# Performance work log

Measured on AMD Instinct MI355X. Metric: run time of the kernel, lower is better.

Reference implementation:

```python
import jax, jax.numpy as jnp
import numpy as np

T, N, I, R, O = 512, 1024, 64, 256, 1  # inter_size == recurrent_size == R


def setup_inputs() -> dict:
    key = jax.random.key(0)
    ks = jax.random.split(key, 13)
    s = 0.05
    return {
        "inputs": jax.random.normal(ks[0], (T, N, I), dtype=jnp.float32),
        # hiddenPrep: Linear(R, R)
        "Whp": jax.random.normal(ks[1], (R, R), jnp.float32) * s,
        "bhp": jax.random.normal(ks[2], (R,), jnp.float32) * s,
        # currentPrep: Linear(I, R)  (inter_size == R)
        "Wcp": jax.random.normal(ks[3], (I, R), jnp.float32) * s,
        "bcp": jax.random.normal(ks[4], (R,), jnp.float32) * s,
        # meshup: Linear(2R, R)
        "Wm": jax.random.normal(ks[5], (2 * R, R), jnp.float32) * s,
        "bm": jax.random.normal(ks[6], (R,), jnp.float32) * s,
        # hiddenPost: Linear(R, R)
        "Whpost": jax.random.normal(ks[7], (R, R), jnp.float32) * s,
        "bhpost": jax.random.normal(ks[8], (R,), jnp.float32) * s,
        "Wr1": jax.random.normal(ks[9], (R, R), jnp.float32) * s,
        "br1": jax.random.normal(ks[10], (R,), jnp.float32) * s,
        "Wr2": jax.random.normal(ks[11], (R, O), jnp.float32) * s,
        "br2": jax.random.normal(ks[12], (O,), jnp.float32) * s,
    }


def reference(inputs, Whp, bhp, Wcp, bcp, Wm, bm, Whpost, bhpost, Wr1, br1, Wr2, br2):
    n, r = inputs.shape[1], Whp.shape[0]

    def step(h, x):
        # RCell_complex: tanh(hiddenPost(tanh(meshup(tanh(cat[hiddenPrep(h), currentPrep(x)])))))
        cat = jnp.tanh(jnp.concatenate([h @ Whp + bhp, x @ Wcp + bcp], axis=-1))  # [N, 2R]
        h_new = jnp.tanh(jnp.tanh(cat @ Wm + bm) @ Whpost + bhpost)  # [N, R]
        out = jax.nn.relu(h_new @ Wr1 + br1) @ Wr2 + br2  # [N, O]
        return h_new, out

    h0 = jnp.zeros((n, r), dtype=inputs.dtype)
    _, outs = jax.lax.scan(step, h0, inputs)  # outs: [T, N, O]
    return outs
```

## Files before the change

kernel.cpp:

```cpp
#include <hip/hip_runtime.h>
#include <hip/hip_bf16.h>

#define TT 512
#define NB 1024

typedef float f32x4 __attribute__((ext_vector_type(4)));
typedef __bf16 bf16x8 __attribute__((ext_vector_type(8)));

#define OFF_HP 0
#define OFF_CP 65536
#define OFF_M  81920
#define OFF_PO 212992
#define OFF_R1 278528
#define TOT    344064

#define H_OFF_BYTES (1u << 20)
#define H_ELEMS ((size_t)TT * 64 * 8 * 512)

#define KEEP(v) asm volatile("" : "+v"(v))

__device__ __forceinline__ bf16x8 as_bf(const f32x4 v) {
  union U { f32x4 f; bf16x8 b; } u; u.f = v; return u.b;
}

__global__ __launch_bounds__(256) void pack_weights(
    const float* __restrict__ Whp, const float* __restrict__ Wm,
    const float* __restrict__ Wcp, const float* __restrict__ Whpost,
    const float* __restrict__ Wr1, __bf16* __restrict__ wsp) {
  int id = blockIdx.x * 256 + threadIdx.x;
  if (id >= TOT) return;
  int j = id & 7, lane = (id >> 3) & 63;
  int lq = lane >> 4, l15 = lane & 15;
  int rel, KT; const float* W; bool perm = true;
  if (id < OFF_CP)      { rel = id;          KT = 8;  W = Whp; }
  else if (id < OFF_M)  { rel = id - OFF_CP; KT = 2;  W = Wcp; perm = false; }
  else if (id < OFF_PO) { rel = id - OFF_M;  KT = 16; W = Wm; }
  else if (id < OFF_R1) { rel = id - OFF_PO; KT = 8;  W = Whpost; }
  else                  { rel = id - OFF_R1; KT = 8;  W = Wr1; }
  int ktm = rel >> 9;
  int kt = ktm % KT, mt = ktm / KT;
  int phi = 16 * mt + l15;
  int kk;
  if (perm) {
    int kb = (kt >= 8) ? kt - 8 : kt;
    kk = 32 * kb + 16 * (j >> 2) + 4 * lq + (j & 3);
    if (kt >= 8) kk += 256;
  } else {
    kk = 32 * kt + 8 * lq + j;
  }
  wsp[id] = (__bf16)W[kk * 256 + phi];
}

__device__ __forceinline__ float tanh_fast(float x) {
  float t = __expf(2.0f * x);
  return 1.0f - __fdividef(2.0f, t + 1.0f);
}

#define MFMA(a, b, c) __builtin_amdgcn_mfma_f32_16x16x32_bf16((a), (b), (c), 0, 0, 0)

__device__ __forceinline__ bf16x8 pack2(__bf16* region, int wv, int lane,
                                        const f32x4& a0, const f32x4& a1) {
  bf16x8 f;
  #pragma unroll
  for (int r = 0; r < 4; ++r) {
    f[r]     = (__bf16)tanh_fast(a0[r]);
    f[4 + r] = (__bf16)tanh_fast(a1[r]);
  }
  *(bf16x8*)(region + wv * 512 + lane * 8) = f;
  return f;
}

__device__ __forceinline__ void barrier_lds() {
  asm volatile("s_waitcnt lgkmcnt(0)" ::: "memory");
  __builtin_amdgcn_s_barrier();
  asm volatile("" ::: "memory");
}

__global__ __launch_bounds__(512)
__attribute__((amdgpu_waves_per_eu(2, 2)))
void rnn_seq_a(
    const float* __restrict__ x, const __bf16* __restrict__ wsp,
    __bf16* __restrict__ hist,
    const float* __restrict__ bhp, const float* __restrict__ bcp,
    const float* __restrict__ bm, const float* __restrict__ bhpost) {
  __shared__ __align__(16) __bf16 hB[8 * 512];
  __shared__ __align__(16) __bf16 mB[16 * 512];
  __shared__ __align__(16) __bf16 uB[8 * 512];
  __shared__ __align__(16) __bf16 wmcL[112 * 512];
  __shared__ float lb[4 * 256];

  const int tid  = threadIdx.x;
  const int wv   = tid >> 6;
  const int lane = tid & 63;
  const int lq   = lane >> 4, l15 = lane & 15;
  const int n0   = blockIdx.x * 16;
  const int mt0  = 2 * wv;

  if (tid < 256) {
    lb[0 * 256 + tid] = bhp[tid];
    lb[1 * 256 + tid] = bcp[tid];
    lb[2 * 256 + tid] = bm[tid];
    lb[3 * 256 + tid] = bhpost[tid];
  }
  for (int i = tid; i < 8 * 512; i += 512) hB[i] = (__bf16)0.0f;

  for (int v = tid; v < 112 * 64; v += 512) {
    int frag = v >> 6, lp = v & 63;
    int mt = frag / 7, c = frag - mt * 7;
    ((bf16x8*)wmcL)[v] =
        *(const bf16x8*)(wsp + OFF_M + (size_t)(mt * 16 + 8 + c) * 512 + lp * 8);
  }

  #define BIAS(a, m) (*(const f32x4*)(lb + (a) * 256 + (m) * 16 + 4 * lq))

  f32x4 hpw[16], wmh[16];
  {
    const __bf16* hp0 = wsp + OFF_HP + (size_t)(mt0 * 8) * 512 + lane * 8;
    const __bf16* mp  = wsp + OFF_M + (size_t)(mt0 * 16) * 512 + lane * 8;
    #pragma unroll
    for (int i = 0; i < 16; ++i) hpw[i] = *(const f32x4*)(hp0 + i * 512);
    #pragma unroll
    for (int kt = 0; kt < 8; ++kt) {
      wmh[kt]     = *(const f32x4*)(mp + kt * 512);
      wmh[8 + kt] = *(const f32x4*)(mp + (16 + kt) * 512);
    }
  }
  #pragma unroll
  for (int i = 0; i < 16; ++i) { KEEP(hpw[i]); KEEP(wmh[i]); }

  const __bf16* cp_p   = wsp + OFF_CP + (size_t)(mt0 * 2) * 512 + lane * 8;
  const __bf16* po_p   = wsp + OFF_PO + (size_t)(mt0 * 8) * 512 + lane * 8;
  const __bf16* wmk15a = wsp + OFF_M + (size_t)(mt0 * 16 + 15) * 512 + lane * 8;
  const __bf16* wmk15b = wsp + OFF_M + (size_t)((mt0 + 1) * 16 + 15) * 512 + lane * 8;
  const __bf16* wc0 = wmcL + (size_t)(mt0 * 7) * 512 + lane * 8;
  const __bf16* wc1 = wmcL + (size_t)((mt0 + 1) * 7) * 512 + lane * 8;
  __bf16* hst = hist + (size_t)(blockIdx.x * 8 + wv) * 512 + lane * 8;

  __syncthreads();

  const float* xbase = x + (size_t)(n0 + l15) * 64 + 8 * lq;
  f32x4 xr0 = *(const f32x4*)(xbase);
  f32x4 xr1 = *(const f32x4*)(xbase + 4);
  f32x4 xr2 = *(const f32x4*)(xbase + 32);
  f32x4 xr3 = *(const f32x4*)(xbase + 36);

  for (int t = 0; t < TT; ++t) {
    bf16x8 Bx0, Bx1;
    #pragma unroll
    for (int j = 0; j < 4; ++j) {
      Bx0[j] = (__bf16)xr0[j]; Bx0[4 + j] = (__bf16)xr1[j];
      Bx1[j] = (__bf16)xr2[j]; Bx1[4 + j] = (__bf16)xr3[j];
    }

    bf16x8 cpb[4];
    #pragma unroll
    for (int p = 0; p < 4; ++p) cpb[p] = *(const bf16x8*)(cp_p + p * 512);
    bf16x8 wk15a = *(const bf16x8*)(wmk15a);
    bf16x8 wk15b = *(const bf16x8*)(wmk15b);
    bf16x8 Bh[8];
    #pragma unroll
    for (int kt = 0; kt < 8; ++kt)
      Bh[kt] = *(const bf16x8*)(hB + kt * 512 + lane * 8);

    f32x4 ah0 = BIAS(0, mt0), ah1 = BIAS(0, mt0 + 1);
    #pragma unroll
    for (int i = 0; i < 16; ++i) {
      bf16x8 a = as_bf(hpw[i]);
      if (i < 8) ah0 = MFMA(a, Bh[i & 7], ah0);
      else       ah1 = MFMA(a, Bh[i & 7], ah1);
    }
    f32x4 ac0 = BIAS(1, mt0), ac1 = BIAS(1, mt0 + 1);
    ac0 = MFMA(cpb[0], Bx0, ac0); ac0 = MFMA(cpb[1], Bx1, ac0);
    ac1 = MFMA(cpb[2], Bx0, ac1); ac1 = MFMA(cpb[3], Bx1, ac1);

    pack2(mB,           wv, lane, ah0, ah1);
    pack2(mB + 8 * 512, wv, lane, ac0, ac1);
    barrier_lds();

    f32x4 am0 = BIAS(2, mt0), am1 = BIAS(2, mt0 + 1);
    #pragma unroll
    for (int i = 0; i < 16; ++i) {
      bf16x8 Bm = *(const bf16x8*)(mB + i * 512 + lane * 8);
      bf16x8 w0, w1;
      if (i < 8)       { w0 = as_bf(wmh[i]); w1 = as_bf(wmh[8 + i]); }
      else if (i < 15) { w0 = *(const bf16x8*)(wc0 + (i - 8) * 512);
                         w1 = *(const bf16x8*)(wc1 + (i - 8) * 512); }
      else             { w0 = wk15a; w1 = wk15b; }
      am0 = MFMA(w0, Bm, am0);
      am1 = MFMA(w1, Bm, am1);
    }
    bf16x8 pob[8];
    #pragma unroll
    for (int p = 0; p < 8; ++p) pob[p] = *(const bf16x8*)(po_p + p * 512);
    {
      int tn = (t + 1 < TT) ? t + 1 : TT - 1;
      const float* xp = xbase + (size_t)tn * NB * 64;
      xr0 = *(const f32x4*)(xp);      xr1 = *(const f32x4*)(xp + 4);
      xr2 = *(const f32x4*)(xp + 32); xr3 = *(const f32x4*)(xp + 36);
    }
    pack2(uB, wv, lane, am0, am1);
    barrier_lds();

    bf16x8 Bu[8];
    #pragma unroll
    for (int kt = 0; kt < 8; ++kt)
      Bu[kt] = *(const bf16x8*)(uB + kt * 512 + lane * 8);
    f32x4 ap0 = BIAS(3, mt0), ap1 = BIAS(3, mt0 + 1);
    #pragma unroll
    for (int i = 0; i < 16; ++i) {
      bf16x8 a = pob[i & 7];
      if (i < 8) ap0 = MFMA(a, Bu[i & 7], ap0);
      else       ap1 = MFMA(a, Bu[i & 7], ap1);
      if (i + 8 < 16) pob[i & 7] = *(const bf16x8*)(po_p + (i + 8) * 512);
    }
    bf16x8 f = pack2(hB, wv, lane, ap0, ap1);
    *(bf16x8*)(hst + (size_t)t * (64 * 8 * 512)) = f;
    barrier_lds();
  }
  #undef BIAS
}

__global__ __launch_bounds__(512) void head_out(
    const __bf16* __restrict__ wsp, const __bf16* __restrict__ hist,
    const float* __restrict__ br1, const float* __restrict__ Wr2,
    const float* __restrict__ br2, float* __restrict__ out) {
  __shared__ float outp[128];
  const int tid  = threadIdx.x;
  const int wv   = tid >> 6;
  const int lane = tid & 63;
  const int lq   = lane >> 4;
  const int t    = blockIdx.x;
  const int mt0  = 2 * wv;

  f32x4 r1w[16];
  {
    const __bf16* r1p = wsp + OFF_R1 + (size_t)(mt0 * 8) * 512 + lane * 8;
    #pragma unroll
    for (int i = 0; i < 16; ++i) r1w[i] = *(const f32x4*)(r1p + i * 512);
  }
  #pragma unroll
  for (int i = 0; i < 16; ++i) KEEP(r1w[i]);

  const f32x4 w2a = *(const f32x4*)(Wr2 + mt0 * 16 + 4 * lq);
  const f32x4 w2b = *(const f32x4*)(Wr2 + (mt0 + 1) * 16 + 4 * lq);
  const f32x4 b0  = *(const f32x4*)(br1 + mt0 * 16 + 4 * lq);
  const f32x4 b1  = *(const f32x4*)(br1 + (mt0 + 1) * 16 + 4 * lq);
  const float br2v = br2[0];

  for (int nb = 0; nb < 64; ++nb) {
    const __bf16* hp = hist + (size_t)((t * 64 + nb) * 8) * 512 + lane * 8;
    bf16x8 Bh[8];
    #pragma unroll
    for (int k = 0; k < 8; ++k) Bh[k] = *(const bf16x8*)(hp + k * 512);
    f32x4 ar0 = b0, ar1 = b1;
    #pragma unroll
    for (int i = 0; i < 16; ++i) {
      if (i < 8) ar0 = MFMA(as_bf(r1w[i]), Bh[i], ar0);
      else       ar1 = MFMA(as_bf(r1w[i]), Bh[i - 8], ar1);
    }
    float p = 0.f;
    #pragma unroll
    for (int r = 0; r < 4; ++r)
      p += fmaxf(ar0[r], 0.f) * w2a[r] + fmaxf(ar1[r], 0.f) * w2b[r];
    p += __shfl_xor(p, 16, 64);
    p += __shfl_xor(p, 32, 64);
    if (lane < 16) outp[wv * 16 + lane] = p;
    __syncthreads();
    if (tid < 16) {
      float s = br2v;
      #pragma unroll
      for (int w = 0; w < 8; ++w) s += outp[w * 16 + tid];
      out[(size_t)t * NB + nb * 16 + tid] = s;
    }
    __syncthreads();
  }
}

__global__ __launch_bounds__(512)
__attribute__((amdgpu_waves_per_eu(2, 2)))
void rnn_seq(
    const float* __restrict__ x, const __bf16* __restrict__ wsp,
    const float* __restrict__ bhp, const float* __restrict__ bcp,
    const float* __restrict__ bm, const float* __restrict__ bhpost,
    const float* __restrict__ br1, const float* __restrict__ Wr2,
    const float* __restrict__ br2, float* __restrict__ out) {
  __shared__ __align__(16) __bf16 hB[8 * 512];
  __shared__ __align__(16) __bf16 mB[16 * 512];
  __shared__ __align__(16) __bf16 uB[8 * 512];
  __shared__ __align__(16) __bf16 r1L[112 * 512];
  __shared__ float lb[5 * 256];
  __shared__ float outp[128];

  const int tid  = threadIdx.x;
  const int wv   = tid >> 6;
  const int lane = tid & 63;
  const int lq   = lane >> 4, l15 = lane & 15;
  const int n0   = blockIdx.x * 16;
  const int mt0  = 2 * wv;

  if (tid < 256) {
    lb[0 * 256 + tid] = bhp[tid];
    lb[1 * 256 + tid] = bcp[tid];
    lb[2 * 256 + tid] = bm[tid];
    lb[3 * 256 + tid] = bhpost[tid];
    lb[4 * 256 + tid] = br1[tid];
  }
  for (int i = tid; i < 8 * 512; i += 512) hB[i] = (__bf16)0.0f;

  for (int v = tid; v < 112 * 64; v += 512) {
    int frag = v >> 6, lp = v & 63;
    int mt = frag / 7, kt = frag - mt * 7;
    ((bf16x8*)r1L)[v] =
        *(const bf16x8*)(wsp + OFF_R1 + (size_t)(mt * 8 + kt) * 512 + lp * 8);
  }
  const float br2v = br2[0];

  #define BIAS(a, m) (*(const f32x4*)(lb + (a) * 256 + (m) * 16 + 4 * lq))
  const f32x4 w2a = *(const f32x4*)(Wr2 + mt0 * 16 + 4 * lq);
  const f32x4 w2b = *(const f32x4*)(Wr2 + (mt0 + 1) * 16 + 4 * lq);

  f32x4 wm0f[16]; bf16x8 wm1[16];
  {
    const __bf16* mp = wsp + OFF_M + (size_t)(mt0 * 16) * 512 + lane * 8;
    #pragma unroll
    for (int kt = 0; kt < 16; ++kt) {
      wm0f[kt] = *(const f32x4*)(mp + kt * 512);
      wm1[kt]  = *(const bf16x8*)(mp + (16 + kt) * 512);
    }
  }
  #pragma unroll
  for (int i = 0; i < 16; ++i) KEEP(wm0f[i]);

  const __bf16* hp_p = wsp + OFF_HP + (size_t)(mt0 * 8) * 512 + lane * 8;
  const __bf16* r1_p = wsp + OFF_R1 + (size_t)(mt0 * 8) * 512 + lane * 8;
  const __bf16* cp_p = wsp + OFF_CP + (size_t)(mt0 * 2) * 512 + lane * 8;
  const __bf16* po_p = wsp + OFF_PO + (size_t)(mt0 * 8) * 512 + lane * 8;
  const __bf16* r1Lp = r1L + (size_t)(mt0 * 7) * 512 + lane * 8;

  __syncthreads();

  const float* xbase = x + (size_t)(n0 + l15) * 64 + 8 * lq;
  f32x4 xr0 = *(const f32x4*)(xbase);
  f32x4 xr1 = *(const f32x4*)(xbase + 4);
  f32x4 xr2 = *(const f32x4*)(xbase + 32);
  f32x4 xr3 = *(const f32x4*)(xbase + 36);

  bf16x8 hpb[8];
  #pragma unroll
  for (int p = 0; p < 8; ++p) hpb[p] = *(const bf16x8*)(hp_p + p * 512);

  for (int t = 0; t < TT; ++t) {
    if (t >= 2 && tid < 16) {
      float s = br2v;
      #pragma unroll
      for (int w = 0; w < 8; ++w) s += outp[w * 16 + tid];
      out[(size_t)(t - 2) * NB + n0 + tid] = s;
    }

    bf16x8 Bx0, Bx1;
    #pragma unroll
    for (int j = 0; j < 4; ++j) {
      Bx0[j] = (__bf16)xr0[j]; Bx0[4 + j] = (__bf16)xr1[j];
      Bx1[j] = (__bf16)xr2[j]; Bx1[4 + j] = (__bf16)xr3[j];
    }

    bf16x8 cpb[4];
    #pragma unroll
    for (int p = 0; p < 4; ++p) cpb[p] = *(const bf16x8*)(cp_p + p * 512);
    bf16x8 r1k7a = *(const bf16x8*)(r1_p + 7 * 512);
    bf16x8 r1k7b = *(const bf16x8*)(r1_p + 15 * 512);
    bf16x8 Bh[8];
    #pragma unroll
    for (int kt = 0; kt < 8; ++kt)
      Bh[kt] = *(const bf16x8*)(hB + kt * 512 + lane * 8);

    f32x4 ah0 = BIAS(0, mt0), ah1 = BIAS(0, mt0 + 1);
    #pragma unroll
    for (int i = 0; i < 16; ++i) {
      bf16x8 a = hpb[i & 7];
      if (i < 8) ah0 = MFMA(a, Bh[i & 7], ah0);
      else       ah1 = MFMA(a, Bh[i & 7], ah1);
      if (i + 8 < 16) hpb[i & 7] = *(const bf16x8*)(hp_p + (i + 8) * 512);
    }
    f32x4 ac0 = BIAS(1, mt0), ac1 = BIAS(1, mt0 + 1);
    ac0 = MFMA(cpb[0], Bx0, ac0); ac0 = MFMA(cpb[1], Bx1, ac0);
    ac1 = MFMA(cpb[2], Bx0, ac1); ac1 = MFMA(cpb[3], Bx1, ac1);

    pack2(mB,           wv, lane, ah0, ah1);
    pack2(mB + 8 * 512, wv, lane, ac0, ac1);
    barrier_lds();

    f32x4 am0 = BIAS(2, mt0), am1 = BIAS(2, mt0 + 1);
    f32x4 ar0 = BIAS(4, mt0), ar1 = BIAS(4, mt0 + 1);
    #pragma unroll
    for (int i = 0; i < 16; ++i) {
      bf16x8 Bm = *(const bf16x8*)(mB + i * 512 + lane * 8);
      am0 = MFMA(as_bf(wm0f[i]), Bm, am0);
      am1 = MFMA(wm1[i], Bm, am1);
      int k = i & 7;
      bf16x8 a;
      if (k < 7) a = *(const bf16x8*)(r1Lp + ((i >> 3) * 7 + k) * 512);
      else       a = (i < 8) ? r1k7a : r1k7b;
      if (i < 8) ar0 = MFMA(a, Bh[k], ar0);
      else       ar1 = MFMA(a, Bh[k], ar1);
    }
    bf16x8 pob[8];
    #pragma unroll
    for (int p = 0; p < 8; ++p) pob[p] = *(const bf16x8*)(po_p + p * 512);
    {
      int tn = (t + 1 < TT) ? t + 1 : TT - 1;
      const float* xp = xbase + (size_t)tn * NB * 64;
      xr0 = *(const f32x4*)(xp);      xr1 = *(const f32x4*)(xp + 4);
      xr2 = *(const f32x4*)(xp + 32); xr3 = *(const f32x4*)(xp + 36);
    }
    pack2(uB, wv, lane, am0, am1);
    barrier_lds();

    #pragma unroll
    for (int p = 0; p < 8; ++p) hpb[p] = *(const bf16x8*)(hp_p + p * 512);
    bf16x8 Bu[8];
    #pragma unroll
    for (int kt = 0; kt < 8; ++kt)
      Bu[kt] = *(const bf16x8*)(uB + kt * 512 + lane * 8);
    {
      float p = 0.f;
      #pragma unroll
      for (int r = 0; r < 4; ++r)
        p += fmaxf(ar0[r], 0.f) * w2a[r] + fmaxf(ar1[r], 0.f) * w2b[r];
      p += __shfl_xor(p, 16, 64);
      p += __shfl_xor(p, 32, 64);
      if (lane < 16) outp[wv * 16 + lane] = p;
    }
    f32x4 ap0 = BIAS(3, mt0), ap1 = BIAS(3, mt0 + 1);
    #pragma unroll
    for (int i = 0; i < 16; ++i) {
      bf16x8 a = pob[i & 7];
      if (i < 8) ap0 = MFMA(a, Bu[i & 7], ap0);
      else       ap1 = MFMA(a, Bu[i & 7], ap1);
      if (i + 8 < 16) pob[i & 7] = *(const bf16x8*)(po_p + (i + 8) * 512);
    }
    pack2(hB, wv, lane, ap0, ap1);
    barrier_lds();
  }

  if (tid < 16) {
    float s = br2v;
    #pragma unroll
    for (int w = 0; w < 8; ++w) s += outp[w * 16 + tid];
    out[(size_t)(TT - 2) * NB + n0 + tid] = s;
  }
  barrier_lds();

  {
    bf16x8 Bh[8];
    #pragma unroll
    for (int kt = 0; kt < 8; ++kt)
      Bh[kt] = *(const bf16x8*)(hB + kt * 512 + lane * 8);
    f32x4 ar0 = BIAS(4, mt0), ar1 = BIAS(4, mt0 + 1);
    bf16x8 r1b[8];
    #pragma unroll
    for (int p = 0; p < 8; ++p) r1b[p] = *(const bf16x8*)(r1_p + p * 512);
    #pragma unroll
    for (int i = 0; i < 16; ++i) {
      bf16x8 a = r1b[i & 7];
      if (i < 8) ar0 = MFMA(a, Bh[i & 7], ar0);
      else       ar1 = MFMA(a, Bh[i & 7], ar1);
      if (i + 8 < 16) r1b[i & 7] = *(const bf16x8*)(r1_p + (i + 8) * 512);
    }
    float p = 0.f;
    #pragma unroll
    for (int r = 0; r < 4; ++r)
      p += fmaxf(ar0[r], 0.f) * w2a[r] + fmaxf(ar1[r], 0.f) * w2b[r];
    p += __shfl_xor(p, 16, 64);
    p += __shfl_xor(p, 32, 64);
    if (lane < 16) outp[wv * 16 + lane] = p;
    barrier_lds();
    if (tid < 16) {
      float s = br2v;
      #pragma unroll
      for (int w = 0; w < 8; ++w) s += outp[w * 16 + tid];
      out[(size_t)(TT - 1) * NB + n0 + tid] = s;
    }
  }
  #undef BIAS
}

extern "C" void kernel_launch(void* const* d_in, const int* in_sizes, int n_in,
                              void* d_out, int out_size, void* d_ws, size_t ws_size,
                              hipStream_t stream) {
  const float* x      = (const float*)d_in[0];
  const float* Whp    = (const float*)d_in[1];
  const float* bhp    = (const float*)d_in[2];
  const float* Wcp    = (const float*)d_in[3];
  const float* bcp    = (const float*)d_in[4];
  const float* Wm     = (const float*)d_in[5];
  const float* bm     = (const float*)d_in[6];
  const float* Whpost = (const float*)d_in[7];
  const float* bhpost = (const float*)d_in[8];
  const float* Wr1    = (const float*)d_in[9];
  const float* br1    = (const float*)d_in[10];
  const float* Wr2    = (const float*)d_in[11];
  const float* br2    = (const float*)d_in[12];
  __bf16* wsp = (__bf16*)d_ws;
  float*  out = (float*)d_out;

  if (ws_size < (size_t)TOT * sizeof(__bf16)) return;

  pack_weights<<<(TOT + 255) / 256, 256, 0, stream>>>(Whp, Wm, Wcp, Whpost, Wr1, wsp);

  const size_t H_BYTES = H_ELEMS * sizeof(__bf16);
  if (ws_size >= (size_t)H_OFF_BYTES + H_BYTES) {
    __bf16* hist = (__bf16*)((char*)d_ws + H_OFF_BYTES);
    rnn_seq_a<<<64, 512, 0, stream>>>(x, wsp, hist, bhp, bcp, bm, bhpost);
    head_out<<<TT, 512, 0, stream>>>(wsp, hist, br1, Wr2, br2, out);
  } else {
    rnn_seq<<<64, 512, 0, stream>>>(x, wsp, bhp, bcp, bm, bhpost, br1, Wr2,
                                    br2, out);
  }
}
```

Before: 2.832 ms.

## Halve recurrent block to 4 waves holding all weights in registers; split head grid

The sequential RNN kernel now runs with 256 threads, and each wave computes four output tiles instead of two. All hiddenPrep, meshup and currentPrep weight fragments are kept in registers (about 416 VGPRs' worth, using AGPRs), which removes the LDS-resident meshup weights and the per-step global weight loads. Each h/m/x fragment read from LDS is also reused across four MFMAs. The head kernel gets a second grid dimension so each block handles a quarter of the batch, and the fallback kernel's prefetch is moved. The trade-off is fewer waves for latency hiding, heavy register pressure and possible spills.

Result: slower. 4.964 ms (+75.3%).

```diff
diff --git a/kernel.cpp b/kernel.cpp
--- a/kernel.cpp
+++ b/kernel.cpp
@@ -58,7 +58,7 @@
 
 #define MFMA(a, b, c) __builtin_amdgcn_mfma_f32_16x16x32_bf16((a), (b), (c), 0, 0, 0)
 
-__device__ __forceinline__ bf16x8 pack2(__bf16* region, int wv, int lane,
+__device__ __forceinline__ bf16x8 pack2(__bf16* region, int fr, int lane,
                                         const f32x4& a0, const f32x4& a1) {
   bf16x8 f;
   #pragma unroll
@@ -66,7 +66,7 @@
     f[r]     = (__bf16)tanh_fast(a0[r]);
     f[4 + r] = (__bf16)tanh_fast(a1[r]);
   }
-  *(bf16x8*)(region + wv * 512 + lane * 8) = f;
+  *(bf16x8*)(region + fr * 512 + lane * 8) = f;
   return f;
 }
 
@@ -76,9 +76,9 @@
   asm volatile("" ::: "memory");
 }
 
-__global__ __launch_bounds__(512)
-__attribute__((amdgpu_waves_per_eu(2, 2)))
-void rnn_seq_a(
+__global__ __launch_bounds__(256)
+__attribute__((amdgpu_waves_per_eu(1, 1)))
+void rnn_seq_c(
     const float* __restrict__ x, const __bf16* __restrict__ wsp,
     __bf16* __restrict__ hist,
     const float* __restrict__ bhp, const float* __restrict__ bcp,
@@ -86,7 +86,6 @@
   __shared__ __align__(16) __bf16 hB[8 * 512];
   __shared__ __align__(16) __bf16 mB[16 * 512];
   __shared__ __align__(16) __bf16 uB[8 * 512];
-  __shared__ __align__(16) __bf16 wmcL[112 * 512];
   __shared__ float lb[4 * 256];
 
   const int tid  = threadIdx.x;
@@ -94,7 +93,8 @@
   const int lane = tid & 63;
   const int lq   = lane >> 4, l15 = lane & 15;
   const int n0   = blockIdx.x * 16;
-  const int mt0  = 2 * wv;
+  const int mt0  = 4 * wv;
+  const int f0   = 2 * wv;
 
   if (tid < 256) {
     lb[0 * 256 + tid] = bhp[tid];
@@ -102,39 +102,34 @@
     lb[2 * 256 + tid] = bm[tid];
     lb[3 * 256 + tid] = bhpost[tid];
   }
-  for (int i = tid; i < 8 * 512; i += 512) hB[i] = (__bf16)0.0f;
-
-  for (int v = tid; v < 112 * 64; v += 512) {
-    int frag = v >> 6, lp = v & 63;
-    int mt = frag / 7, c = frag - mt * 7;
-    ((bf16x8*)wmcL)[v] =
-        *(const bf16x8*)(wsp + OFF_M + (size_t)(mt * 16 + 8 + c) * 512 + lp * 8);
-  }
+  for (int i = tid; i < 8 * 512; i += 256) hB[i] = (__bf16)0.0f;
 
   #define BIAS(a, m) (*(const f32x4*)(lb + (a) * 256 + (m) * 16 + 4 * lq))
 
-  f32x4 hpw[16], wmh[16];
+  f32x4 hpw[32], wmw[64], cpw[8];
   {
-    const __bf16* hp0 = wsp + OFF_HP + (size_t)(mt0 * 8) * 512 + lane * 8;
-    const __bf16* mp  = wsp + OFF_M + (size_t)(mt0 * 16) * 512 + lane * 8;
-    #pragma unroll
-    for (int i = 0; i < 16; ++i) hpw[i] = *(const f32x4*)(hp0 + i * 512);
-    #pragma unroll
-    for (int kt = 0; kt < 8; ++kt) {
-      wmh[kt]     = *(const f32x4*)(mp + kt * 512);
-      wmh[8 + kt] = *(const f32x4*)(mp + (16 + kt) * 512);
-    }
-  }
-  #pragma unroll
-  for (int i = 0; i < 16; ++i) { KEEP(hpw[i]); KEEP(wmh[i]); }
-
-  const __bf16* cp_p   = wsp + OFF_CP + (size_t)(mt0 * 2) * 512 + lane * 8;
-  const __bf16* po_p   = wsp + OFF_PO + (size_t)(mt0 * 8) * 512 + lane * 8;
-  const __bf16* wmk15a = wsp + OFF_M + (size_t)(mt0 * 16 + 15) * 512 + lane * 8;
-  const __bf16* wmk15b = wsp + OFF_M + (size_t)((mt0 + 1) * 16 + 15) * 512 + lane * 8;
-  const __bf16* wc0 = wmcL + (size_t)(mt0 * 7) * 512 + lane * 8;
-  const __bf16* wc1 = wmcL + (size_t)((mt0 + 1) * 7) * 512 + lane * 8;
-  __bf16* hst = hist + (size_t)(blockIdx.x * 8 + wv) * 512 + lane * 8;
+    #pragma unroll
+    for (int mt = 0; mt < 4; ++mt) {
+      const __bf16* hp0 = wsp + OFF_HP + (size_t)((mt0 + mt) * 8) * 512 + lane * 8;
+      const __bf16* mm0 = wsp + OFF_M  + (size_t)((mt0 + mt) * 16) * 512 + lane * 8;
+      const __bf16* cc0 = wsp + OFF_CP + (size_t)((mt0 + mt) * 2) * 512 + lane * 8;
+      #pragma unroll
+      for (int kt = 0; kt < 8; ++kt)  hpw[mt * 8 + kt]  = *(const f32x4*)(hp0 + kt * 512);
+      #pragma unroll
+      for (int i = 0; i < 16; ++i)    wmw[mt * 16 + i]  = *(const f32x4*)(mm0 + i * 512);
+      #pragma unroll
+      for (int k = 0; k < 2; ++k)     cpw[mt * 2 + k]   = *(const f32x4*)(cc0 + k * 512);
+    }
+  }
+  #pragma unroll
+  for (int i = 0; i < 32; ++i) KEEP(hpw[i]);
+  #pragma unroll
+  for (int i = 0; i < 64; ++i) KEEP(wmw[i]);
+  #pragma unroll
+  for (int i = 0; i < 8; ++i)  KEEP(cpw[i]);
+
+  const __bf16* po_p = wsp + OFF_PO + (size_t)(mt0 * 8) * 512 + lane * 8;
+  __bf16* hst = hist + (size_t)(blockIdx.x * 8 + f0) * 512 + lane * 8;
 
   __syncthreads();
 
@@ -152,69 +147,78 @@
       Bx1[j] = (__bf16)xr2[j]; Bx1[4 + j] = (__bf16)xr3[j];
     }
 
-    bf16x8 cpb[4];
-    #pragma unroll
-    for (int p = 0; p < 4; ++p) cpb[p] = *(const bf16x8*)(cp_p + p * 512);
-    bf16x8 wk15a = *(const bf16x8*)(wmk15a);
-    bf16x8 wk15b = *(const bf16x8*)(wmk15b);
-    bf16x8 Bh[8];
-    #pragma unroll
-    for (int kt = 0; kt < 8; ++kt)
-      Bh[kt] = *(const bf16x8*)(hB + kt * 512 + lane * 8);
-
-    f32x4 ah0 = BIAS(0, mt0), ah1 = BIAS(0, mt0 + 1);
-    #pragma unroll
-    for (int i = 0; i < 16; ++i) {
-      bf16x8 a = as_bf(hpw[i]);
-      if (i < 8) ah0 = MFMA(a, Bh[i & 7], ah0);
-      else       ah1 = MFMA(a, Bh[i & 7], ah1);
-    }
-    f32x4 ac0 = BIAS(1, mt0), ac1 = BIAS(1, mt0 + 1);
-    ac0 = MFMA(cpb[0], Bx0, ac0); ac0 = MFMA(cpb[1], Bx1, ac0);
-    ac1 = MFMA(cpb[2], Bx0, ac1); ac1 = MFMA(cpb[3], Bx1, ac1);
-
-    pack2(mB,           wv, lane, ah0, ah1);
-    pack2(mB + 8 * 512, wv, lane, ac0, ac1);
-    barrier_lds();
-
-    f32x4 am0 = BIAS(2, mt0), am1 = BIAS(2, mt0 + 1);
-    #pragma unroll
-    for (int i = 0; i < 16; ++i) {
-      bf16x8 Bm = *(const bf16x8*)(mB + i * 512 + lane * 8);
-      bf16x8 w0, w1;
-      if (i < 8)       { w0 = as_bf(wmh[i]); w1 = as_bf(wmh[8 + i]); }
-      else if (i < 15) { w0 = *(const bf16x8*)(wc0 + (i - 8) * 512);
-                         w1 = *(const bf16x8*)(wc1 + (i - 8) * 512); }
-      else             { w0 = wk15a; w1 = wk15b; }
-      am0 = MFMA(w0, Bm, am0);
-      am1 = MFMA(w1, Bm, am1);
-    }
+    f32x4 ah[4];
+    #pragma unroll
+    for (int mt = 0; mt < 4; ++mt) ah[mt] = BIAS(0, mt0 + mt);
+    #pragma unroll
+    for (int kt = 0; kt < 8; ++kt) {
+      bf16x8 bh = *(const bf16x8*)(hB + kt * 512 + lane * 8);
+      #pragma unroll
+      for (int mt = 0; mt < 4; ++mt)
+        ah[mt] = MFMA(as_bf(hpw[mt * 8 + kt]), bh, ah[mt]);
+    }
+    f32x4 ac[4];
+    #pragma unroll
+    for (int mt = 0; mt < 4; ++mt) {
+      ac[mt] = BIAS(1, mt0 + mt);
+      ac[mt] = MFMA(as_bf(cpw[mt * 2 + 0]), Bx0, ac[mt]);
+      ac[mt] = MFMA(as_bf(cpw[mt * 2 + 1]), Bx1, ac[mt]);
+    }
+    pack2(mB,           f0,     lane, ah[0], ah[1]);
+    pack2(mB,           f0 + 1, lane, ah[2], ah[3]);
+    pack2(mB + 8 * 512, f0,     lane, ac[0], ac[1]);
+    pack2(mB + 8 * 512, f0 + 1, lane, ac[2], ac[3]);
+    barrier_lds();
+
     bf16x8 pob[8];
     #pragma unroll
-    for (int p = 0; p < 8; ++p) pob[p] = *(const bf16x8*)(po_p + p * 512);
+    for (int c = 0; c < 8; ++c) {
+      int g = (c & 3) * 8 + (c >> 2);
+      pob[c] = *(const bf16x8*)(po_p + g * 512);
+    }
     {
       int tn = (t + 1 < TT) ? t + 1 : TT - 1;
       const float* xp = xbase + (size_t)tn * NB * 64;
       xr0 = *(const f32x4*)(xp);      xr1 = *(const f32x4*)(xp + 4);
       xr2 = *(const f32x4*)(xp + 32); xr3 = *(const f32x4*)(xp + 36);
     }
-    pack2(uB, wv, lane, am0, am1);
-    barrier_lds();
-
-    bf16x8 Bu[8];
-    #pragma unroll
-    for (int kt = 0; kt < 8; ++kt)
-      Bu[kt] = *(const bf16x8*)(uB + kt * 512 + lane * 8);
-    f32x4 ap0 = BIAS(3, mt0), ap1 = BIAS(3, mt0 + 1);
+    f32x4 am[4];
+    #pragma unroll
+    for (int mt = 0; mt < 4; ++mt) am[mt] = BIAS(2, mt0 + mt);
     #pragma unroll
     for (int i = 0; i < 16; ++i) {
-      bf16x8 a = pob[i & 7];
-      if (i < 8) ap0 = MFMA(a, Bu[i & 7], ap0);
-      else       ap1 = MFMA(a, Bu[i & 7], ap1);
-      if (i + 8 < 16) pob[i & 7] = *(const bf16x8*)(po_p + (i + 8) * 512);
-    }
-    bf16x8 f = pack2(hB, wv, lane, ap0, ap1);
-    *(bf16x8*)(hst + (size_t)t * (64 * 8 * 512)) = f;
+      bf16x8 bmv = *(const bf16x8*)(mB + i * 512 + lane * 8);
+      #pragma unroll
+      for (int mt = 0; mt < 4; ++mt)
+        am[mt] = MFMA(as_bf(wmw[mt * 16 + i]), bmv, am[mt]);
+    }
+    pack2(uB, f0,     lane, am[0], am[1]);
+    pack2(uB, f0 + 1, lane, am[2], am[3]);
+    barrier_lds();
+
+    f32x4 ap[4];
+    #pragma unroll
+    for (int mt = 0; mt < 4; ++mt) ap[mt] = BIAS(3, mt0 + mt);
+    #pragma unroll
+    for (int kt = 0; kt < 8; ++kt) {
+      bf16x8 bu = *(const bf16x8*)(uB + kt * 512 + lane * 8);
+      #pragma unroll
+      for (int mt = 0; mt < 4; ++mt) {
+        int c = kt * 4 + mt;
+        ap[mt] = MFMA(pob[c & 7], bu, ap[mt]);
+        if (c + 8 < 32) {
+          int g = ((c + 8) & 3) * 8 + ((c + 8) >> 2);
+          pob[c & 7] = *(const bf16x8*)(po_p + g * 512);
+        }
+      }
+    }
+    bf16x8 h0 = pack2(hB, f0,     lane, ap[0], ap[1]);
+    bf16x8 h1 = pack2(hB, f0 + 1, lane, ap[2], ap[3]);
+    {
+      __bf16* hw = hst + (size_t)t * (64 * 8 * 512);
+      *(bf16x8*)(hw)       = h0;
+      *(bf16x8*)(hw + 512) = h1;
+    }
     barrier_lds();
   }
   #undef BIAS
@@ -230,6 +234,7 @@
   const int lane = tid & 63;
   const int lq   = lane >> 4;
   const int t    = blockIdx.x;
+  const int nb0  = blockIdx.y * 16;
   const int mt0  = 2 * wv;
 
   f32x4 r1w[16];
@@ -247,7 +252,7 @@
   const f32x4 b1  = *(const f32x4*)(br1 + (mt0 + 1) * 16 + 4 * lq);
   const float br2v = br2[0];
 
-  for (int nb = 0; nb < 64; ++nb) {
+  for (int nb = nb0; nb < nb0 + 16; ++nb) {
     const __bf16* hp = hist + (size_t)((t * 64 + nb) * 8) * 512 + lane * 8;
     bf16x8 Bh[8];
     #pragma unroll
@@ -416,8 +421,6 @@
     pack2(uB, wv, lane, am0, am1);
     barrier_lds();
 
-    #pragma unroll
-    for (int p = 0; p < 8; ++p) hpb[p] = *(const bf16x8*)(hp_p + p * 512);
     bf16x8 Bu[8];
     #pragma unroll
     for (int kt = 0; kt < 8; ++kt)
@@ -440,6 +443,8 @@
       if (i + 8 < 16) pob[i & 7] = *(const bf16x8*)(po_p + (i + 8) * 512);
     }
     pack2(hB, wv, lane, ap0, ap1);
+    #pragma unroll
+    for (int p = 0; p < 8; ++p) hpb[p] = *(const bf16x8*)(hp_p + p * 512);
     barrier_lds();
   }
 
@@ -511,8 +516,8 @@
   const size_t H_BYTES = H_ELEMS * sizeof(__bf16);
   if (ws_size >= (size_t)H_OFF_BYTES + H_BYTES) {
     __bf16* hist = (__bf16*)((char*)d_ws + H_OFF_BYTES);
-    rnn_seq_a<<<64, 512, 0, stream>>>(x, wsp, hist, bhp, bcp, bm, bhpost);
-    head_out<<<TT, 512, 0, stream>>>(wsp, hist, br1, Wr2, br2, out);
+    rnn_seq_c<<<64, 256, 0, stream>>>(x, wsp, hist, bhp, bcp, bm, bhpost);
+    head_out<<<dim3(TT, 4), 512, 0, stream>>>(wsp, hist, br1, Wr2, br2, out);
   } else {
     rnn_seq<<<64, 512, 0, stream>>>(x, wsp, bhp, bcp, bm, bhpost, br1, Wr2,
                                     br2, out);
```

## Double-buffer head loads, widen head grid, and hoist hiddenPost weight loads

Applied to the files above, without the earlier changes.

The head kernel now splits each timestep's 64 batch tiles across 8 blocks in a second grid dimension. Each block double-buffers its hidden-state loads so the next tile's global reads overlap the current tile's MFMA work. In the recurrent kernel, all 16 hiddenPost weight fragments are fetched earlier (half before the meshup MFMAs) instead of being streamed inside the MFMA loop, which raises register pressure. The fallback kernel moves its hiddenPrep weight reload to before the final barrier.

Result: slower. 2.984 ms (+5.4%).

```diff
diff --git a/kernel.cpp b/kernel.cpp
--- a/kernel.cpp
+++ b/kernel.cpp
@@ -58,7 +58,7 @@
 
 #define MFMA(a, b, c) __builtin_amdgcn_mfma_f32_16x16x32_bf16((a), (b), (c), 0, 0, 0)
 
-__device__ __forceinline__ bf16x8 pack2(__bf16* region, int wv, int lane,
+__device__ __forceinline__ bf16x8 pack2(__bf16* region, int fr, int lane,
                                         const f32x4& a0, const f32x4& a1) {
   bf16x8 f;
   #pragma unroll
@@ -66,7 +66,7 @@
     f[r]     = (__bf16)tanh_fast(a0[r]);
     f[4 + r] = (__bf16)tanh_fast(a1[r]);
   }
-  *(bf16x8*)(region + wv * 512 + lane * 8) = f;
+  *(bf16x8*)(region + fr * 512 + lane * 8) = f;
   return f;
 }
 
@@ -177,6 +177,10 @@
     pack2(mB + 8 * 512, wv, lane, ac0, ac1);
     barrier_lds();
 
+    bf16x8 pob[16];
+    #pragma unroll
+    for (int p = 0; p < 8; ++p) pob[p] = *(const bf16x8*)(po_p + p * 512);
+
     f32x4 am0 = BIAS(2, mt0), am1 = BIAS(2, mt0 + 1);
     #pragma unroll
     for (int i = 0; i < 16; ++i) {
@@ -189,9 +193,8 @@
       am0 = MFMA(w0, Bm, am0);
       am1 = MFMA(w1, Bm, am1);
     }
-    bf16x8 pob[8];
-    #pragma unroll
-    for (int p = 0; p < 8; ++p) pob[p] = *(const bf16x8*)(po_p + p * 512);
+    #pragma unroll
+    for (int p = 8; p < 16; ++p) pob[p] = *(const bf16x8*)(po_p + p * 512);
     {
       int tn = (t + 1 < TT) ? t + 1 : TT - 1;
       const float* xp = xbase + (size_t)tn * NB * 64;
@@ -208,10 +211,9 @@
     f32x4 ap0 = BIAS(3, mt0), ap1 = BIAS(3, mt0 + 1);
     #pragma unroll
     for (int i = 0; i < 16; ++i) {
-      bf16x8 a = pob[i & 7];
+      bf16x8 a = pob[i];
       if (i < 8) ap0 = MFMA(a, Bu[i & 7], ap0);
       else       ap1 = MFMA(a, Bu[i & 7], ap1);
-      if (i + 8 < 16) pob[i & 7] = *(const bf16x8*)(po_p + (i + 8) * 512);
     }
     bf16x8 f = pack2(hB, wv, lane, ap0, ap1);
     *(bf16x8*)(hst + (size_t)t * (64 * 8 * 512)) = f;
@@ -230,6 +232,7 @@
   const int lane = tid & 63;
   const int lq   = lane >> 4;
   const int t    = blockIdx.x;
+  const int nb0  = blockIdx.y * 8;
   const int mt0  = 2 * wv;
 
   f32x4 r1w[16];
@@ -247,33 +250,48 @@
   const f32x4 b1  = *(const f32x4*)(br1 + (mt0 + 1) * 16 + 4 * lq);
   const float br2v = br2[0];
 
-  for (int nb = 0; nb < 64; ++nb) {
-    const __bf16* hp = hist + (size_t)((t * 64 + nb) * 8) * 512 + lane * 8;
-    bf16x8 Bh[8];
-    #pragma unroll
-    for (int k = 0; k < 8; ++k) Bh[k] = *(const bf16x8*)(hp + k * 512);
-    f32x4 ar0 = b0, ar1 = b1;
-    #pragma unroll
-    for (int i = 0; i < 16; ++i) {
-      if (i < 8) ar0 = MFMA(as_bf(r1w[i]), Bh[i], ar0);
-      else       ar1 = MFMA(as_bf(r1w[i]), Bh[i - 8], ar1);
-    }
-    float p = 0.f;
-    #pragma unroll
-    for (int r = 0; r < 4; ++r)
-      p += fmaxf(ar0[r], 0.f) * w2a[r] + fmaxf(ar1[r], 0.f) * w2b[r];
-    p += __shfl_xor(p, 16, 64);
-    p += __shfl_xor(p, 32, 64);
-    if (lane < 16) outp[wv * 16 + lane] = p;
-    __syncthreads();
-    if (tid < 16) {
-      float s = br2v;
-      #pragma unroll
-      for (int w = 0; w < 8; ++w) s += outp[w * 16 + tid];
-      out[(size_t)t * NB + nb * 16 + tid] = s;
-    }
-    __syncthreads();
-  }
+  const __bf16* hb = hist + (size_t)(t * 64) * 8 * 512 + lane * 8;
+
+  #define LOADH(dst, nb)                                                    \
+    { const __bf16* hp_ = hb + (size_t)(nb) * 8 * 512;                      \
+      _Pragma("unroll")                                                     \
+      for (int k_ = 0; k_ < 8; ++k_)                                        \
+        dst[k_] = *(const bf16x8*)(hp_ + k_ * 512); }
+
+  #define COMPUTE(src, nb)                                                  \
+    { f32x4 ar0 = b0, ar1 = b1;                                             \
+      _Pragma("unroll")                                                     \
+      for (int i_ = 0; i_ < 16; ++i_) {                                     \
+        if (i_ < 8) ar0 = MFMA(as_bf(r1w[i_]), src[i_], ar0);               \
+        else        ar1 = MFMA(as_bf(r1w[i_]), src[i_ - 8], ar1);           \
+      }                                                                     \
+      float p_ = 0.f;                                                       \
+      _Pragma("unroll")                                                     \
+      for (int r_ = 0; r_ < 4; ++r_)                                        \
+        p_ += fmaxf(ar0[r_], 0.f) * w2a[r_] + fmaxf(ar1[r_], 0.f) * w2b[r_];\
+      p_ += __shfl_xor(p_, 16, 64);                                         \
+      p_ += __shfl_xor(p_, 32, 64);                                         \
+      if (lane < 16) outp[wv * 16 + lane] = p_;                             \
+      barrier_lds();                                                        \
+      if (tid < 16) {                                                       \
+        float s_ = br2v;                                                    \
+        _Pragma("unroll")                                                   \
+        for (int w_ = 0; w_ < 8; ++w_) s_ += outp[w_ * 16 + tid];           \
+        out[(size_t)t * NB + (nb) * 16 + tid] = s_;                         \
+      }                                                                     \
+      barrier_lds(); }
+
+  bf16x8 BA[8], BB[8];
+  LOADH(BA, nb0);
+  #pragma unroll
+  for (int k = 0; k < 8; k += 2) {
+    LOADH(BB, nb0 + k + 1);
+    COMPUTE(BA, nb0 + k);
+    LOADH(BA, (k + 2 < 8) ? nb0 + k + 2 : nb0);
+    COMPUTE(BB, nb0 + k + 1);
+  }
+  #undef LOADH
+  #undef COMPUTE
 }
 
 __global__ __launch_bounds__(512)
@@ -416,8 +434,6 @@
     pack2(uB, wv, lane, am0, am1);
     barrier_lds();
 
-    #pragma unroll
-    for (int p = 0; p < 8; ++p) hpb[p] = *(const bf16x8*)(hp_p + p * 512);
     bf16x8 Bu[8];
     #pragma unroll
     for (int kt = 0; kt < 8; ++kt)
@@ -440,6 +456,8 @@
       if (i + 8 < 16) pob[i & 7] = *(const bf16x8*)(po_p + (i + 8) * 512);
     }
     pack2(hB, wv, lane, ap0, ap1);
+    #pragma unroll
+    for (int p = 0; p < 8; ++p) hpb[p] = *(const bf16x8*)(hp_p + p * 512);
     barrier_lds();
   }
 
@@ -512,7 +530,7 @@
   if (ws_size >= (size_t)H_OFF_BYTES + H_BYTES) {
     __bf16* hist = (__bf16*)((char*)d_ws + H_OFF_BYTES);
     rnn_seq_a<<<64, 512, 0, stream>>>(x, wsp, hist, bhp, bcp, bm, bhpost);
-    head_out<<<TT, 512, 0, stream>>>(wsp, hist, br1, Wr2, br2, out);
+    head_out<<<dim3(TT, 8), 512, 0, stream>>>(wsp, hist, br1, Wr2, br2, out);
   } else {
     rnn_seq<<<64, 512, 0, stream>>>(x, wsp, bhp, bcp, bm, bhpost, br1, Wr2,
                                     br2, out);
```

## Fuse output head into recurrent kernel as per-block epilogue over history

Applied to the files above, without the earlier changes.

Removes the separate head_out launch. Each recurrent block now waits for its own history writes, then runs the regressor head over its 16-column slice for all timesteps, two steps per iteration. This saves a kernel launch and the 512-block head pass, but the head runs on only 64 blocks, which may serialize work that was previously spread across many CUs. It also moves the hiddenPrep weight prefetch in the fallback kernel to after the hidden-state store.

Result: slower. 3.470 ms (+22.5%).

```diff
diff --git a/kernel.cpp b/kernel.cpp
--- a/kernel.cpp
+++ b/kernel.cpp
@@ -16,6 +16,7 @@
 
 #define H_OFF_BYTES (1u << 20)
 #define H_ELEMS ((size_t)TT * 64 * 8 * 512)
+#define HSTEP   ((size_t)64 * 8 * 512)
 
 #define KEEP(v) asm volatile("" : "+v"(v))
 
@@ -58,7 +59,7 @@
 
 #define MFMA(a, b, c) __builtin_amdgcn_mfma_f32_16x16x32_bf16((a), (b), (c), 0, 0, 0)
 
-__device__ __forceinline__ bf16x8 pack2(__bf16* region, int wv, int lane,
+__device__ __forceinline__ bf16x8 pack2(__bf16* region, int fr, int lane,
                                         const f32x4& a0, const f32x4& a1) {
   bf16x8 f;
   #pragma unroll
@@ -66,7 +67,7 @@
     f[r]     = (__bf16)tanh_fast(a0[r]);
     f[4 + r] = (__bf16)tanh_fast(a1[r]);
   }
-  *(bf16x8*)(region + wv * 512 + lane * 8) = f;
+  *(bf16x8*)(region + fr * 512 + lane * 8) = f;
   return f;
 }
 
@@ -82,12 +83,15 @@
     const float* __restrict__ x, const __bf16* __restrict__ wsp,
     __bf16* __restrict__ hist,
     const float* __restrict__ bhp, const float* __restrict__ bcp,
-    const float* __restrict__ bm, const float* __restrict__ bhpost) {
+    const float* __restrict__ bm, const float* __restrict__ bhpost,
+    const float* __restrict__ br1, const float* __restrict__ Wr2,
+    const float* __restrict__ br2, float* __restrict__ out) {
   __shared__ __align__(16) __bf16 hB[8 * 512];
   __shared__ __align__(16) __bf16 mB[16 * 512];
   __shared__ __align__(16) __bf16 uB[8 * 512];
   __shared__ __align__(16) __bf16 wmcL[112 * 512];
   __shared__ float lb[4 * 256];
+  __shared__ float outp[128], outp2[128];
 
   const int tid  = threadIdx.x;
   const int wv   = tid >> 6;
@@ -214,23 +218,13 @@
       if (i + 8 < 16) pob[i & 7] = *(const bf16x8*)(po_p + (i + 8) * 512);
     }
     bf16x8 f = pack2(hB, wv, lane, ap0, ap1);
-    *(bf16x8*)(hst + (size_t)t * (64 * 8 * 512)) = f;
-    barrier_lds();
-  }
-  #undef BIAS
-}
-
-__global__ __launch_bounds__(512) void head_out(
-    const __bf16* __restrict__ wsp, const __bf16* __restrict__ hist,
-    const float* __restrict__ br1, const float* __restrict__ Wr2,
-    const float* __restrict__ br2, float* __restrict__ out) {
-  __shared__ float outp[128];
-  const int tid  = threadIdx.x;
-  const int wv   = tid >> 6;
-  const int lane = tid & 63;
-  const int lq   = lane >> 4;
-  const int t    = blockIdx.x;
-  const int mt0  = 2 * wv;
+    *(bf16x8*)(hst + (size_t)t * HSTEP) = f;
+    barrier_lds();
+  }
+
+  asm volatile("s_waitcnt vmcnt(0)" ::: "memory");
+  __builtin_amdgcn_s_barrier();
+  asm volatile("" ::: "memory");
 
   f32x4 r1w[16];
   {
@@ -238,42 +232,69 @@
     #pragma unroll
     for (int i = 0; i < 16; ++i) r1w[i] = *(const f32x4*)(r1p + i * 512);
   }
-  #pragma unroll
-  for (int i = 0; i < 16; ++i) KEEP(r1w[i]);
-
   const f32x4 w2a = *(const f32x4*)(Wr2 + mt0 * 16 + 4 * lq);
   const f32x4 w2b = *(const f32x4*)(Wr2 + (mt0 + 1) * 16 + 4 * lq);
-  const f32x4 b0  = *(const f32x4*)(br1 + mt0 * 16 + 4 * lq);
-  const f32x4 b1  = *(const f32x4*)(br1 + (mt0 + 1) * 16 + 4 * lq);
+  const f32x4 rb0 = *(const f32x4*)(br1 + mt0 * 16 + 4 * lq);
+  const f32x4 rb1 = *(const f32x4*)(br1 + (mt0 + 1) * 16 + 4 * lq);
   const float br2v = br2[0];
 
-  for (int nb = 0; nb < 64; ++nb) {
-    const __bf16* hp = hist + (size_t)((t * 64 + nb) * 8) * 512 + lane * 8;
-    bf16x8 Bh[8];
-    #pragma unroll
-    for (int k = 0; k < 8; ++k) Bh[k] = *(const bf16x8*)(hp + k * 512);
-    f32x4 ar0 = b0, ar1 = b1;
-    #pragma unroll
-    for (int i = 0; i < 16; ++i) {
-      if (i < 8) ar0 = MFMA(as_bf(r1w[i]), Bh[i], ar0);
-      else       ar1 = MFMA(as_bf(r1w[i]), Bh[i - 8], ar1);
-    }
-    float p = 0.f;
-    #pragma unroll
-    for (int r = 0; r < 4; ++r)
-      p += fmaxf(ar0[r], 0.f) * w2a[r] + fmaxf(ar1[r], 0.f) * w2b[r];
-    p += __shfl_xor(p, 16, 64);
-    p += __shfl_xor(p, 32, 64);
-    if (lane < 16) outp[wv * 16 + lane] = p;
-    __syncthreads();
+  const __bf16* hrd = hist + (size_t)(blockIdx.x * 8) * 512 + lane * 8;
+
+  for (int t = 0; t < TT; t += 2) {
+    float pv0, pv1;
+    {
+      const __bf16* hp = hrd + (size_t)t * HSTEP;
+      bf16x8 Bh[8];
+      #pragma unroll
+      for (int k = 0; k < 8; ++k) Bh[k] = *(const bf16x8*)(hp + k * 512);
+      f32x4 ar0 = rb0, ar1 = rb1;
+      #pragma unroll
+      for (int i = 0; i < 16; ++i) {
+        if (i < 8) ar0 = MFMA(as_bf(r1w[i]), Bh[i], ar0);
+        else       ar1 = MFMA(as_bf(r1w[i]), Bh[i - 8], ar1);
+      }
+      float p = 0.f;
+      #pragma unroll
+      for (int r = 0; r < 4; ++r)
+        p += fmaxf(ar0[r], 0.f) * w2a[r] + fmaxf(ar1[r], 0.f) * w2b[r];
+      p += __shfl_xor(p, 16, 64);
+      p += __shfl_xor(p, 32, 64);
+      pv0 = p;
+    }
+    {
+      const __bf16* hp = hrd + (size_t)(t + 1) * HSTEP;
+      bf16x8 Bh[8];
+      #pragma unroll
+      for (int k = 0; k < 8; ++k) Bh[k] = *(const bf16x8*)(hp + k * 512);
+      f32x4 ar0 = rb0, ar1 = rb1;
+      #pragma unroll
+      for (int i = 0; i < 16; ++i) {
+        if (i < 8) ar0 = MFMA(as_bf(r1w[i]), Bh[i], ar0);
+        else       ar1 = MFMA(as_bf(r1w[i]), Bh[i - 8], ar1);
+      }
+      float p = 0.f;
+      #pragma unroll
+      for (int r = 0; r < 4; ++r)
+        p += fmaxf(ar0[r], 0.f) * w2a[r] + fmaxf(ar1[r], 0.f) * w2b[r];
+      p += __shfl_xor(p, 16, 64);
+      p += __shfl_xor(p, 32, 64);
+      pv1 = p;
+    }
+    if (lane < 16) { outp[wv * 16 + lane] = pv0; outp2[wv * 16 + lane] = pv1; }
+    barrier_lds();
     if (tid < 16) {
-      float s = br2v;
-      #pragma unroll
-      for (int w = 0; w < 8; ++w) s += outp[w * 16 + tid];
-      out[(size_t)t * NB + nb * 16 + tid] = s;
-    }
-    __syncthreads();
-  }
+      float s0 = br2v, s1 = br2v;
+      #pragma unroll
+      for (int w = 0; w < 8; ++w) {
+        s0 += outp[w * 16 + tid];
+        s1 += outp2[w * 16 + tid];
+      }
+      out[(size_t)t * NB + n0 + tid]       = s0;
+      out[(size_t)(t + 1) * NB + n0 + tid] = s1;
+    }
+    barrier_lds();
+  }
+  #undef BIAS
 }
 
 __global__ __launch_bounds__(512)
@@ -416,8 +437,6 @@
     pack2(uB, wv, lane, am0, am1);
     barrier_lds();
 
-    #pragma unroll
-    for (int p = 0; p < 8; ++p) hpb[p] = *(const bf16x8*)(hp_p + p * 512);
     bf16x8 Bu[8];
     #pragma unroll
     for (int kt = 0; kt < 8; ++kt)
@@ -440,6 +459,8 @@
       if (i + 8 < 16) pob[i & 7] = *(const bf16x8*)(po_p + (i + 8) * 512);
     }
     pack2(hB, wv, lane, ap0, ap1);
+    #pragma unroll
+    for (int p = 0; p < 8; ++p) hpb[p] = *(const bf16x8*)(hp_p + p * 512);
     barrier_lds();
   }
 
@@ -511,8 +532,8 @@
   const size_t H_BYTES = H_ELEMS * sizeof(__bf16);
   if (ws_size >= (size_t)H_OFF_BYTES + H_BYTES) {
     __bf16* hist = (__bf16*)((char*)d_ws + H_OFF_BYTES);
-    rnn_seq_a<<<64, 512, 0, stream>>>(x, wsp, hist, bhp, bcp, bm, bhpost);
-    head_out<<<TT, 512, 0, stream>>>(wsp, hist, br1, Wr2, br2, out);
+    rnn_seq_a<<<64, 512, 0, stream>>>(x, wsp, hist, bhp, bcp, bm, bhpost,
+                                      br1, Wr2, br2, out);
   } else {
     rnn_seq<<<64, 512, 0, stream>>>(x, wsp, bhp, bcp, bm, bhpost, br1, Wr2,
                                     br2, out);
```
